# Kernel optimization log

Measured on AMD Instinct MI355X. Metric: run time of the kernel, lower is better.

Reference implementation:

```python
import jax, jax.numpy as jnp
import numpy as np

N_PANO, N_FP = 50000, 10000
D_IN, D_FP, HID, OUT = 128, 64, 128, 64
E_PP, E_PF = 800000, 50000


def _gat(x_src, x_dst, src, dst, Ws, Wd, a_s, a_d, b, n_dst):
    # PyG GATConv (heads=1, add_self_loops=False, bipartite lin_src/lin_dst)
    hs = x_src @ Ws                      # [Ns, C]
    hd = x_dst @ Wd                      # [Nd, C]
    es = hs @ a_s                        # [Ns]
    ed = hd @ a_d                        # [Nd]
    e = jax.nn.leaky_relu(es[src] + ed[dst], negative_slope=0.2)  # [E]
    m = jax.ops.segment_max(e, dst, num_segments=n_dst)
    ex = jnp.exp(e - m[dst])
    den = jax.ops.segment_sum(ex, dst, num_segments=n_dst)
    alpha = ex / den[dst]                # segment softmax over incoming edges
    out = jax.ops.segment_sum(hs[src] * alpha[:, None], dst, num_segments=n_dst)
    return out + b


def setup_inputs() -> dict:
    key = jax.random.key(0)
    ks = jax.random.split(key, 32)
    s_in = 1.0 / np.sqrt(D_IN)
    s_hid = 1.0 / np.sqrt(HID)
    s_fp = 1.0 / np.sqrt(D_FP)
    inp = {
        "x_pano": jax.random.normal(ks[0], (N_PANO, D_IN), jnp.float32),
        "x_fp": jax.random.normal(ks[1], (N_FP, D_FP), jnp.float32),
        # layer 0 (in = D_IN)
        "Ws0": jax.random.normal(ks[2], (D_IN, HID)) * s_in,
        "Wd0": jax.random.normal(ks[3], (D_IN, HID)) * s_in,
        "as0": jax.random.normal(ks[4], (HID,)) * 0.1,
        "ad0": jax.random.normal(ks[5], (HID,)) * 0.1,
        "b0": jnp.zeros((HID,), jnp.float32),
        "Lw0": jax.random.normal(ks[6], (D_IN, HID)) * s_in,
        "Lb0": jnp.zeros((HID,), jnp.float32),
        # layer 1 (in = HID)
        "Ws1": jax.random.normal(ks[7], (HID, HID)) * s_hid,
        "Wd1": jax.random.normal(ks[8], (HID, HID)) * s_hid,
        "as1": jax.random.normal(ks[9], (HID,)) * 0.1,
        "ad1": jax.random.normal(ks[10], (HID,)) * 0.1,
        "b1": jnp.zeros((HID,), jnp.float32),
        "Lw1": jax.random.normal(ks[11], (HID, HID)) * s_hid,
        "Lb1": jnp.zeros((HID,), jnp.float32),
        # translate conv pano -> footprint
        "Wts": jax.random.normal(ks[12], (HID, OUT)) * s_hid,
        "Wtd": jax.random.normal(ks[13], (D_FP, OUT)) * s_fp,
        "ats": jax.random.normal(ks[14], (OUT,)) * 0.1,
        "atd": jax.random.normal(ks[15], (OUT,)) * 0.1,
        "bt": jnp.zeros((OUT,), jnp.float32),
        "edge_pp": jax.random.randint(ks[16], (2, E_PP), 0, N_PANO),
        "edge_pf_src": jax.random.randint(ks[17], (E_PF,), 0, N_PANO),
        "edge_pf_dst": jax.random.randint(ks[18], (E_PF,), 0, N_FP),
    }
    return inp


def reference(x_pano, x_fp, Ws0, Wd0, as0, ad0, b0, Lw0, Lb0,
              Ws1, Wd1, as1, ad1, b1, Lw1, Lb1,
              Wts, Wtd, ats, atd, bt,
              edge_pp, edge_pf_src, edge_pf_dst):
    src, dst = edge_pp[0], edge_pp[1]
    layer_params = [(Ws0, Wd0, as0, ad0, b0, Lw0, Lb0),
                    (Ws1, Wd1, as1, ad1, b1, Lw1, Lb1)]
    h = x_pano
    for (Ws, Wd, a_s, a_d, b, Lw, Lb) in layer_params:
        conv = _gat(h, h, src, dst, Ws, Wd, a_s, a_d, b, N_PANO)
        h = jax.nn.relu(conv + h @ Lw + Lb)
    # HeteroConv with single relation + aggr='sum' == the bipartite conv output
    out_fp = _gat(h, x_fp, edge_pf_src, edge_pf_dst, Wts, Wtd, ats, atd, bt, N_FP)
    return out_fp
```

## Files before the change

kernel.cpp:

```cpp
#include <hip/hip_runtime.h>
#include <hip/hip_bf16.h>
#include <math.h>

#define N_PANO 50000
#define N_FP   10000
#define N_UNI  60000
#define HID    128
#define OUT_C  64
#define E_PP   800000
#define E_PF   50000
#define E_UNI  850000
#define NBKT   235
#define EPB    4096

typedef unsigned short ushort_t;
typedef unsigned int uint_t;
typedef __attribute__((ext_vector_type(8))) short short8;
typedef __attribute__((ext_vector_type(4))) float f32x4;

static inline int cdiv(int a, int b) { return (a + b - 1) / b; }

__device__ inline ushort_t f2bf(float x) {
    __hip_bfloat16 h = __float2bfloat16(x);
    return *reinterpret_cast<ushort_t*>(&h);
}
__device__ inline float bfu2f(ushort_t u) {
    return __uint_as_float(((uint_t)u) << 16);
}
__device__ inline float bflo(uint_t u) { return __uint_as_float((u & 0xffffu) << 16); }
__device__ inline float bfhi(uint_t u) { return __uint_as_float(u & 0xffff0000u); }
__device__ inline f32x4 mfma16(short8 a, short8 b, f32x4 c) {
    return __builtin_amdgcn_mfma_f32_16x16x32_bf16(a, b, c, 0, 0, 0);
}

__global__ __launch_bounds__(256) void zero_i32(int* p, int n) {
    int i = blockIdx.x * 256 + threadIdx.x;
    if (i < n) p[i] = 0;
}

__global__ __launch_bounds__(256) void bucket_count(const int* __restrict__ pp_dst,
                                                    const int* __restrict__ pf_dst,
                                                    int* __restrict__ bcnt) {
    __shared__ int hist[NBKT];
    const int tid = threadIdx.x;
    const int e0 = blockIdx.x * EPB;
    for (int t = tid; t < NBKT; t += 256) hist[t] = 0;
    __syncthreads();
    #pragma unroll
    for (int u = 0; u < EPB / 256; ++u) {
        int e = e0 + u * 256 + tid;
        int d = -1;
        if (e < E_PP) d = pp_dst[e];
        else if (e < E_UNI) d = N_PANO + pf_dst[e - E_PP];
        if (d >= 0) atomicAdd(&hist[d >> 8], 1);
    }
    __syncthreads();
    for (int t = tid; t < NBKT; t += 256)
        if (hist[t] > 0) atomicAdd(&bcnt[t * 16], hist[t]);
}

__global__ __launch_bounds__(256) void bucket_scan(const int* __restrict__ bcnt,
                                                   int* __restrict__ base, int* __restrict__ bcur) {
    __shared__ int wsum[4];
    int tid = threadIdx.x, lane = tid & 63, wid = tid >> 6;
    int v = (tid < NBKT) ? bcnt[tid * 16] : 0;
    int incl = v;
    #pragma unroll
    for (int off = 1; off < 64; off <<= 1) {
        int t = __shfl_up(incl, off, 64);
        if (lane >= off) incl += t;
    }
    if (lane == 63) wsum[wid] = incl;
    __syncthreads();
    if (tid == 0) {
        int run = 0;
        #pragma unroll
        for (int w = 0; w < 4; ++w) { int t = wsum[w]; wsum[w] = run; run += t; }
    }
    __syncthreads();
    int excl = wsum[wid] + incl - v;
    if (tid < NBKT) { base[tid] = excl; bcur[tid * 16] = excl; }
    if (tid == NBKT) base[NBKT] = E_UNI;
}

__global__ __launch_bounds__(256) void bucket_scatter_uni(const int* __restrict__ pp_src,
                                                          const int* __restrict__ pp_dst,
                                                          const int* __restrict__ pf_src,
                                                          const int* __restrict__ pf_dst,
                                                          int* __restrict__ bcur, int2* __restrict__ tmp) {
    __shared__ int hist[NBKT];
    __shared__ int base[NBKT];
    const int tid = threadIdx.x;
    const int e0 = blockIdx.x * EPB;
    for (int t = tid; t < NBKT; t += 256) hist[t] = 0;
    __syncthreads();
    int d[16], s[16];
    #pragma unroll
    for (int u = 0; u < 16; ++u) {
        int e = e0 + u * 256 + tid;
        if (e < E_PP)       { d[u] = pp_dst[e];                 s[u] = pp_src[e]; }
        else if (e < E_UNI) { d[u] = N_PANO + pf_dst[e - E_PP]; s[u] = pf_src[e - E_PP]; }
        else d[u] = -1;
        if (d[u] >= 0) atomicAdd(&hist[d[u] >> 8], 1);
    }
    __syncthreads();
    for (int t = tid; t < NBKT; t += 256) {
        int c = hist[t];
        base[t] = (c > 0) ? atomicAdd(&bcur[t * 16], c) : 0;
        hist[t] = 0;
    }
    __syncthreads();
    #pragma unroll
    for (int u = 0; u < 16; ++u) {
        if (d[u] >= 0) {
            int b = d[u] >> 8;
            int p = base[b] + atomicAdd(&hist[b], 1);
            tmp[p] = make_int2(s[u], d[u]);
        }
    }
}

__global__ __launch_bounds__(256) void bucket_fine_sort(const int2* __restrict__ tmp,
                                                        const int* __restrict__ base,
                                                        int* __restrict__ ptr, int* __restrict__ col) {
    __shared__ int hist[256];
    __shared__ int wsum[4];
    const int b = blockIdx.x, tid = threadIdx.x, lane = tid & 63, wid = tid >> 6;
    const int B0 = base[b], B1 = base[b + 1];
    hist[tid] = 0;
    __syncthreads();
    for (int e = B0 + tid; e < B1; e += 256) atomicAdd(&hist[tmp[e].y & 255], 1);
    __syncthreads();
    int v = hist[tid];
    int incl = v;
    #pragma unroll
    for (int off = 1; off < 64; off <<= 1) {
        int t = __shfl_up(incl, off, 64);
        if (lane >= off) incl += t;
    }
    if (lane == 63) wsum[wid] = incl;
    __syncthreads();
    if (tid == 0) {
        int run = 0;
        #pragma unroll
        for (int w = 0; w < 4; ++w) { int t = wsum[w]; wsum[w] = run; run += t; }
    }
    __syncthreads();
    int excl = wsum[wid] + incl - v;
    int dg = b * 256 + tid;
    if (dg < N_UNI) ptr[dg] = B0 + excl;
    if (b == NBKT - 1 && tid == 0) ptr[N_UNI] = E_UNI;
    hist[tid] = excl;
    __syncthreads();
    for (int e = B0 + tid; e < B1; e += 256) {
        int2 ed = tmp[e];
        int p = B0 + atomicAdd(&hist[ed.y & 255], 1);
        col[p] = ed.x;
    }
}

__global__ __launch_bounds__(64) void wed_all(const float* __restrict__ Wd0, const float* __restrict__ ad0,
                                              const float* __restrict__ Wd1, const float* __restrict__ ad1,
                                              const float* __restrict__ Wtd, const float* __restrict__ atd,
                                              float* __restrict__ o0, float* __restrict__ o1,
                                              float* __restrict__ ot) {
    int bid = blockIdx.x, lane = threadIdx.x;
    const float* W; const float* a; float* o; int r, C;
    if (bid < 128)      { W = Wd0; a = ad0; o = o0; r = bid;       C = 128; }
    else if (bid < 256) { W = Wd1; a = ad1; o = o1; r = bid - 128; C = 128; }
    else                { W = Wtd; a = atd; o = ot; r = bid - 256; C = 64;  }
    float s = 0.f;
    for (int j = lane; j < C; j += 64) s += W[r * C + j] * a[j];
    #pragma unroll
    for (int off = 32; off; off >>= 1) s += __shfl_down(s, off, 64);
    if (lane == 0) o[r] = s;
}

__global__ __launch_bounds__(256) void wconv(const float* __restrict__ Ws0, const float* __restrict__ Lw0,
                                             const float* __restrict__ Ws1, const float* __restrict__ Lw1,
                                             const float* __restrict__ Wts,
                                             ushort_t* s0, ushort_t* l0, ushort_t* s1, ushort_t* l1,
                                             ushort_t* ts) {
    int i = blockIdx.x * 256 + threadIdx.x;
    const float* W; ushort_t* oh;
    int d, NIc, Cc;
    if (i < 65536) {
        int m = i >> 14; d = i & 16383;
        W = (m == 0) ? Ws0 : (m == 1) ? Lw0 : (m == 2) ? Ws1 : Lw1;
        oh = (m == 0) ? s0 : (m == 1) ? l0 : (m == 2) ? s1 : l1;
        NIc = 8; Cc = 128;
    } else if (i < 73728) {
        d = i - 65536; W = Wts; oh = ts;
        NIc = 4; Cc = 64;
    } else return;
    int j = d & 7, l = (d >> 3) & 63;
    int kcl = (d >> 9) & 1;
    int ni = (d >> 10) & (NIc - 1);
    int p = d >> (10 + (NIc == 8 ? 3 : 2));
    int kc = p * 2 + kcl;
    int n = ni * 16 + (l & 15);
    int k = kc * 32 + (l >> 4) * 8 + j;
    oh[d] = f2bf(W[k * Cc + n]);
}

template <int CN, bool DUAL, bool FP32IN>
__global__ __launch_bounds__(256, 2) void gemm_mfma(const float* __restrict__ Xf,
                                                 const ushort_t* __restrict__ Xh,
                                                 const ushort_t* __restrict__ W1, const ushort_t* __restrict__ W2,
                                                 ushort_t* __restrict__ Y1, ushort_t* __restrict__ Y2,
                                                 const float* __restrict__ avec, float* __restrict__ evec,
                                                 const float* __restrict__ wed, float* __restrict__ edv,
                                                 int N) {
    constexpr int NI = CN / 16;
    constexpr int NMAT = DUAL ? 2 : 1;
    constexpr int SLAB = NI * 1024;
    __shared__ ushort_t Bsh[NMAT * SLAB];
    const int tid = threadIdx.x;
    const int w = tid >> 6, l = tid & 63;
    const int col = l & 15, q = l >> 4;
    const int row0 = blockIdx.x * 128 + w * 32;
    f32x4 acc1[2][NI];
    f32x4 acc2[2][DUAL ? NI : 1];
    #pragma unroll
    for (int m = 0; m < 2; ++m)
        #pragma unroll
        for (int ni = 0; ni < NI; ++ni)
            #pragma unroll
            for (int r = 0; r < 4; ++r) acc1[m][ni][r] = 0.f;
    if (DUAL) {
        #pragma unroll
        for (int m = 0; m < 2; ++m)
            #pragma unroll
            for (int ni = 0; ni < NI; ++ni)
                #pragma unroll
                for (int r = 0; r < 4; ++r) acc2[m][ni][r] = 0.f;
    }
    float ped[2] = {0.f, 0.f};

    #pragma unroll
    for (int p = 0; p < 2; ++p) {
        if (p) __syncthreads();
        {
            const uint4* src1 = (const uint4*)W1 + p * (SLAB / 8);
            uint4* dst1 = (uint4*)&Bsh[0];
            #pragma unroll
            for (int f = tid; f < SLAB / 8; f += 256) dst1[f] = src1[f];
            if (DUAL) {
                const uint4* src2 = (const uint4*)W2 + p * (SLAB / 8);
                uint4* dst2 = (uint4*)&Bsh[SLAB];
                #pragma unroll
                for (int f = tid; f < SLAB / 8; f += 256) dst2[f] = src2[f];
            }
        }
        __syncthreads();
        #pragma unroll
        for (int kcl = 0; kcl < 2; ++kcl) {
            const int kc = p * 2 + kcl;
            const int k0 = kc * 32 + q * 8;
            short8 Ah[2];
            #pragma unroll
            for (int m = 0; m < 2; ++m) {
                const int arow = row0 + m * 16 + col;
                if (FP32IN) {
                    float xv[8];
                    if (arow < N) {
                        float4 a0 = *(const float4*)&Xf[(size_t)arow * 128 + k0];
                        float4 a1 = *(const float4*)&Xf[(size_t)arow * 128 + k0 + 4];
                        xv[0] = a0.x; xv[1] = a0.y; xv[2] = a0.z; xv[3] = a0.w;
                        xv[4] = a1.x; xv[5] = a1.y; xv[6] = a1.z; xv[7] = a1.w;
                    } else {
                        #pragma unroll
                        for (int j = 0; j < 8; ++j) xv[j] = 0.f;
                    }
                    #pragma unroll
                    for (int j = 0; j < 8; ++j) Ah[m][j] = (short)f2bf(xv[j]);
                    if (wed) {
                        float4 w0 = *(const float4*)&wed[k0];
                        float4 w1 = *(const float4*)&wed[k0 + 4];
                        ped[m] += xv[0] * w0.x + xv[1] * w0.y + xv[2] * w0.z + xv[3] * w0.w
                                + xv[4] * w1.x + xv[5] * w1.y + xv[6] * w1.z + xv[7] * w1.w;
                    }
                } else {
                    if (arow < N) {
                        Ah[m] = *(const short8*)&Xh[(size_t)arow * 128 + k0];
                    } else {
                        #pragma unroll
                        for (int j = 0; j < 8; ++j) Ah[m][j] = 0;
                    }
                    if (wed) {
                        float4 w0 = *(const float4*)&wed[k0];
                        float4 w1 = *(const float4*)&wed[k0 + 4];
                        float wv[8] = {w0.x, w0.y, w0.z, w0.w, w1.x, w1.y, w1.z, w1.w};
                        #pragma unroll
                        for (int j = 0; j < 8; ++j)
                            ped[m] += bfu2f((ushort_t)Ah[m][j]) * wv[j];
                    }
                }
            }
            #pragma unroll
            for (int ni = 0; ni < NI; ++ni) {
                const int lb = ((ni * 2 + kcl) * 64 + l) * 8;
                short8 B1 = *(const short8*)&Bsh[lb];
                #pragma unroll
                for (int m = 0; m < 2; ++m) acc1[m][ni] = mfma16(Ah[m], B1, acc1[m][ni]);
                if (DUAL) {
                    short8 B2 = *(const short8*)&Bsh[SLAB + lb];
                    #pragma unroll
                    for (int m = 0; m < 2; ++m) acc2[m][ni] = mfma16(Ah[m], B2, acc2[m][ni]);
                }
            }
        }
    }

    #pragma unroll
    for (int m = 0; m < 2; ++m) {
        #pragma unroll
        for (int ni = 0; ni < NI; ++ni) {
            #pragma unroll
            for (int r = 0; r < 4; ++r) {
                int mrow = row0 + m * 16 + q * 4 + r;
                if (mrow < N) {
                    Y1[(size_t)mrow * CN + ni * 16 + col] = f2bf(acc1[m][ni][r]);
                    if (DUAL) Y2[(size_t)mrow * CN + ni * 16 + col] = f2bf(acc2[m][ni][r]);
                }
            }
        }
    }
    float av[NI];
    #pragma unroll
    for (int ni = 0; ni < NI; ++ni) av[ni] = avec[ni * 16 + col];
    #pragma unroll
    for (int m = 0; m < 2; ++m) {
        #pragma unroll
        for (int r = 0; r < 4; ++r) {
            float pp = 0.f;
            #pragma unroll
            for (int ni = 0; ni < NI; ++ni) pp += acc1[m][ni][r] * av[ni];
            pp += __shfl_xor(pp, 1, 64);
            pp += __shfl_xor(pp, 2, 64);
            pp += __shfl_xor(pp, 4, 64);
            pp += __shfl_xor(pp, 8, 64);
            int mrow = row0 + m * 16 + q * 4 + r;
            if (col == 0 && mrow < N) evec[mrow] = pp;
        }
    }
    if (wed) {
        #pragma unroll
        for (int m = 0; m < 2; ++m) {
            ped[m] += __shfl_xor(ped[m], 16, 64);
            ped[m] += __shfl_xor(ped[m], 32, 64);
            int arow = row0 + m * 16 + col;
            if (q == 0 && arow < N) edv[arow] = ped[m];
        }
    }
}

template <int K>
__global__ __launch_bounds__(256) void matvec_k(const float* __restrict__ X, const float* __restrict__ v,
                                                float* __restrict__ y, int N) {
    int lane = threadIdx.x & 63, wid = threadIdx.x >> 6;
    int node = blockIdx.x * 4 + wid;
    if (node >= N) return;
    float s = X[node * K + lane] * v[lane];
    if (K > 64) s += X[node * K + 64 + lane] * v[64 + lane];
    #pragma unroll
    for (int off = 32; off; off >>= 1) s += __shfl_down(s, off, 64);
    if (lane == 0) y[node] = s;
}

__global__ __launch_bounds__(256) void agg_pano6(const int* __restrict__ ptr, const int* __restrict__ col,
                                                 const float* __restrict__ es, const float* __restrict__ ed,
                                                 const ushort_t* __restrict__ hsb, const ushort_t* __restrict__ linb,
                                                 const float* __restrict__ b, const float* __restrict__ Lb,
                                                 uint_t* __restrict__ hh, int N) {
    int lane = threadIdx.x & 63, wid = threadIdx.x >> 6;
    int node = blockIdx.x * 4 + wid;
    if (node >= N) return;
    int beg = ptr[node], end = ptr[node + 1];
    float edn = ed[node];
    const int half = lane >> 5, hl = lane & 31;
    float a0 = 0.f, a1 = 0.f, a2 = 0.f, a3 = 0.f, denp = 0.f;
    for (int base = beg; base < end; base += 64) {
        int m = min(64, end - base);
        int s = 0;
        float wgt = 0.f;
        if (lane < m) {
            s = col[base + lane];
            float e = es[s] + edn;
            e = fmaxf(e, 0.2f * e);
            wgt = __expf(e);
        }
        denp += wgt;
        int mp = (m + 1) & ~1;
        int t = 0;
        for (; t + 8 <= mp; t += 8) {
            int i0 = t + half, i1 = t + 2 + half, i2 = t + 4 + half, i3 = t + 6 + half;
            int s0 = __shfl(s, i0, 64), s1 = __shfl(s, i1, 64);
            int s2 = __shfl(s, i2, 64), s3 = __shfl(s, i3, 64);
            float w0 = __shfl(wgt, i0, 64), w1 = __shfl(wgt, i1, 64);
            float w2 = __shfl(wgt, i2, 64), w3 = __shfl(wgt, i3, 64);
            uint2 h0 = *(const uint2*)&hsb[(size_t)s0 * 128 + hl * 4];
            uint2 h1 = *(const uint2*)&hsb[(size_t)s1 * 128 + hl * 4];
            uint2 h2 = *(const uint2*)&hsb[(size_t)s2 * 128 + hl * 4];
            uint2 h3 = *(const uint2*)&hsb[(size_t)s3 * 128 + hl * 4];
            a0 += w0 * bflo(h0.x) + w1 * bflo(h1.x) + w2 * bflo(h2.x) + w3 * bflo(h3.x);
            a1 += w0 * bfhi(h0.x) + w1 * bfhi(h1.x) + w2 * bfhi(h2.x) + w3 * bfhi(h3.x);
            a2 += w0 * bflo(h0.y) + w1 * bflo(h1.y) + w2 * bflo(h2.y) + w3 * bflo(h3.y);
            a3 += w0 * bfhi(h0.y) + w1 * bfhi(h1.y) + w2 * bfhi(h2.y) + w3 * bfhi(h3.y);
        }
        for (; t < mp; t += 2) {
            int i0 = t + half;
            int s0 = __shfl(s, i0, 64);
            float w0 = __shfl(wgt, i0, 64);
            uint2 h0 = *(const uint2*)&hsb[(size_t)s0 * 128 + hl * 4];
            a0 += w0 * bflo(h0.x);
            a1 += w0 * bfhi(h0.x);
            a2 += w0 * bflo(h0.y);
            a3 += w0 * bfhi(h0.y);
        }
    }
    a0 += __shfl_xor(a0, 32, 64);
    a1 += __shfl_xor(a1, 32, 64);
    a2 += __shfl_xor(a2, 32, 64);
    a3 += __shfl_xor(a3, 32, 64);
    float den = denp;
    #pragma unroll
    for (int off = 1; off < 64; off <<= 1) den += __shfl_xor(den, off, 64);
    float inv = (end > beg) ? (1.f / den) : 0.f;
    if (half == 0) {
        const ushort_t* lrow = linb + (size_t)node * 128;
        uint2 lv = *(const uint2*)&lrow[hl * 4];
        float4 bb = *(const float4*)&b[hl * 4];
        float4 lb4 = *(const float4*)&Lb[hl * 4];
        float o0 = fmaxf(a0 * inv + bb.x + bflo(lv.x) + lb4.x, 0.f);
        float o1 = fmaxf(a1 * inv + bb.y + bfhi(lv.x) + lb4.y, 0.f);
        float o2 = fmaxf(a2 * inv + bb.z + bflo(lv.y) + lb4.z, 0.f);
        float o3 = fmaxf(a3 * inv + bb.w + bfhi(lv.y) + lb4.w, 0.f);
        uint2 ov;
        ov.x = (uint_t)f2bf(o0) | ((uint_t)f2bf(o1) << 16);
        ov.y = (uint_t)f2bf(o2) | ((uint_t)f2bf(o3) << 16);
        *(uint2*)&hh[(size_t)node * 64 + hl * 2] = ov;
    }
}

__global__ __launch_bounds__(256) void agg_fp4(const int* __restrict__ ptr, const int* __restrict__ col,
                                               const float* __restrict__ es, const float* __restrict__ ed,
                                               const ushort_t* __restrict__ hsb, const float* __restrict__ bt,
                                               float* __restrict__ out, int N) {
    int lane = threadIdx.x & 63, wid = threadIdx.x >> 6;
    int node = blockIdx.x * 4 + wid;
    if (node >= N) return;
    int beg = ptr[node], end = ptr[node + 1];
    float edn = ed[node];
    float acc = 0.f, denp = 0.f;
    for (int base = beg; base < end; base += 64) {
        int m = min(64, end - base);
        int s = 0;
        float wgt = 0.f;
        if (lane < m) {
            s = col[base + lane];
            float e = es[s] + edn;
            e = fmaxf(e, 0.2f * e);
            wgt = __expf(e);
        }
        denp += wgt;
        int u = 0;
        for (; u + 4 <= m; u += 4) {
            int s0 = __shfl(s, u, 64), s1 = __shfl(s, u + 1, 64);
            int s2 = __shfl(s, u + 2, 64), s3 = __shfl(s, u + 3, 64);
            float w0 = __shfl(wgt, u, 64), w1 = __shfl(wgt, u + 1, 64);
            float w2 = __shfl(wgt, u + 2, 64), w3 = __shfl(wgt, u + 3, 64);
            float h0 = bfu2f(hsb[(size_t)s0 * 64 + lane]);
            float h1 = bfu2f(hsb[(size_t)s1 * 64 + lane]);
            float h2 = bfu2f(hsb[(size_t)s2 * 64 + lane]);
            float h3 = bfu2f(hsb[(size_t)s3 * 64 + lane]);
            acc += w0 * h0 + w1 * h1 + w2 * h2 + w3 * h3;
        }
        for (; u < m; ++u) {
            int su = __shfl(s, u, 64);
            float wu = __shfl(wgt, u, 64);
            acc += wu * bfu2f(hsb[(size_t)su * 64 + lane]);
        }
    }
    float den = denp;
    #pragma unroll
    for (int off = 1; off < 64; off <<= 1) den += __shfl_xor(den, off, 64);
    float inv = (end > beg) ? (1.f / den) : 0.f;
    out[(size_t)node * 64 + lane] = acc * inv + bt[lane];
}

extern "C" void kernel_launch(void* const* d_in, const int* in_sizes, int n_in,
                              void* d_out, int out_size, void* d_ws, size_t ws_size,
                              hipStream_t stream) {
    const float* x_pano = (const float*)d_in[0];
    const float* x_fp   = (const float*)d_in[1];
    const float* Ws0 = (const float*)d_in[2];
    const float* Wd0 = (const float*)d_in[3];
    const float* as0 = (const float*)d_in[4];
    const float* ad0 = (const float*)d_in[5];
    const float* b0  = (const float*)d_in[6];
    const float* Lw0 = (const float*)d_in[7];
    const float* Lb0 = (const float*)d_in[8];
    const float* Ws1 = (const float*)d_in[9];
    const float* Wd1 = (const float*)d_in[10];
    const float* as1 = (const float*)d_in[11];
    const float* ad1 = (const float*)d_in[12];
    const float* b1  = (const float*)d_in[13];
    const float* Lw1 = (const float*)d_in[14];
    const float* Lb1 = (const float*)d_in[15];
    const float* Wts = (const float*)d_in[16];
    const float* Wtd = (const float*)d_in[17];
    const float* ats = (const float*)d_in[18];
    const float* atd = (const float*)d_in[19];
    const float* bt  = (const float*)d_in[20];
    const int* edge_pp = (const int*)d_in[21];
    const int* pf_src  = (const int*)d_in[22];
    const int* pf_dst  = (const int*)d_in[23];
    float* out = (float*)d_out;

    char* wsp = (char*)d_ws;
    size_t off = 0;
    auto alloc = [&](size_t bytes) -> char* {
        char* p = wsp + off;
        off += (bytes + 255) & ~(size_t)255;
        return p;
    };
    ushort_t* hsb  = (ushort_t*)alloc(sizeof(ushort_t) * N_PANO * HID);
    ushort_t* linb = (ushort_t*)alloc(sizeof(ushort_t) * N_PANO * HID);
    uint_t* hh     = (uint_t*)alloc(sizeof(uint_t) * N_PANO * 64);
    ushort_t* hstb = (ushort_t*)alloc(sizeof(ushort_t) * N_PANO * OUT_C);
    int2* tmp_e    = (int2*)alloc(sizeof(int2) * E_UNI);
    float* es   = (float*)alloc(sizeof(float) * N_PANO);
    float* ed   = (float*)alloc(sizeof(float) * N_PANO);
    float* edt  = (float*)alloc(sizeof(float) * N_FP);
    float* wed0 = (float*)alloc(sizeof(float) * HID);
    float* wed1 = (float*)alloc(sizeof(float) * HID);
    float* wedt = (float*)alloc(sizeof(float) * OUT_C);
    ushort_t* s0 = (ushort_t*)alloc(sizeof(ushort_t) * 128 * 128);
    ushort_t* l0 = (ushort_t*)alloc(sizeof(ushort_t) * 128 * 128);
    ushort_t* s1 = (ushort_t*)alloc(sizeof(ushort_t) * 128 * 128);
    ushort_t* l1 = (ushort_t*)alloc(sizeof(ushort_t) * 128 * 128);
    ushort_t* ts = (ushort_t*)alloc(sizeof(ushort_t) * 64 * 128);
    int* bcnt   = (int*)alloc(sizeof(int) * NBKT * 16);
    int* bcur   = (int*)alloc(sizeof(int) * NBKT * 16);
    int* bbase  = (int*)alloc(sizeof(int) * (NBKT + 1));
    int* P      = (int*)alloc(sizeof(int) * (N_UNI + 1));
    int* col_u  = (int*)alloc(sizeof(int) * E_UNI);

    const int* pp_src = edge_pp;
    const int* pp_dst = edge_pp + E_PP;

    zero_i32<<<cdiv(NBKT * 16, 256), 256, 0, stream>>>(bcnt, NBKT * 16);
    bucket_count<<<cdiv(E_UNI, EPB), 256, 0, stream>>>(pp_dst, pf_dst, bcnt);
    bucket_scan<<<1, 256, 0, stream>>>(bcnt, bbase, bcur);
    bucket_scatter_uni<<<cdiv(E_UNI, EPB), 256, 0, stream>>>(pp_src, pp_dst, pf_src, pf_dst, bcur, tmp_e);
    bucket_fine_sort<<<NBKT, 256, 0, stream>>>(tmp_e, bbase, P, col_u);

    wed_all<<<320, 64, 0, stream>>>(Wd0, ad0, Wd1, ad1, Wtd, atd, wed0, wed1, wedt);
    wconv<<<288, 256, 0, stream>>>(Ws0, Lw0, Ws1, Lw1, Wts, s0, l0, s1, l1, ts);

    const int gemm_grid = cdiv(N_PANO, 128);

    gemm_mfma<128, true, true><<<gemm_grid, 256, 0, stream>>>(
        x_pano, nullptr, s0, l0, hsb, linb, as0, es, wed0, ed, N_PANO);
    agg_pano6<<<cdiv(N_PANO, 4), 256, 0, stream>>>(P, col_u, es, ed, hsb, linb, b0, Lb0, hh, N_PANO);

    gemm_mfma<128, true, false><<<gemm_grid, 256, 0, stream>>>(
        nullptr, (const ushort_t*)hh, s1, l1, hsb, linb, as1, es, wed1, ed, N_PANO);
    agg_pano6<<<cdiv(N_PANO, 4), 256, 0, stream>>>(P, col_u, es, ed, hsb, linb, b1, Lb1, hh, N_PANO);

    gemm_mfma<64, false, false><<<gemm_grid, 256, 0, stream>>>(
        nullptr, (const ushort_t*)hh, ts, nullptr, hstb, nullptr, ats, es, nullptr, nullptr, N_PANO);
    matvec_k<64><<<cdiv(N_FP, 4), 256, 0, stream>>>(x_fp, wedt, edt, N_FP);
    agg_fp4<<<cdiv(N_FP, 4), 256, 0, stream>>>(P + N_PANO, col_u, es, edt, hstb, bt, out, N_FP);
}
```

Baseline: 282.3 us.

## Process two nodes per wave in pano aggregation and merge prep kernels

The pano aggregation kernel now assigns two destination nodes to each wavefront and interleaves their edge chunks. Each half-wave writes one node's output, which aims to raise memory-level parallelism and cut idle lanes on low-degree nodes. The two weight-prep kernels are merged into one launch. The footprint dst-score matvec is folded into the footprint aggregation kernel, removing one more launch. Handling two nodes per wave raises register pressure and adds serialization when the two nodes have very different degrees.

Measured after the change: 277.8 us. About the same (-1.6%).

```diff
diff --git a/kernel.cpp b/kernel.cpp
--- a/kernel.cpp
+++ b/kernel.cpp
@@ -159,48 +159,51 @@
     }
 }
 
-__global__ __launch_bounds__(64) void wed_all(const float* __restrict__ Wd0, const float* __restrict__ ad0,
+__global__ __launch_bounds__(256) void prep_k(const float* __restrict__ Ws0, const float* __restrict__ Lw0,
+                                              const float* __restrict__ Ws1, const float* __restrict__ Lw1,
+                                              const float* __restrict__ Wts,
+                                              const float* __restrict__ Wd0, const float* __restrict__ ad0,
                                               const float* __restrict__ Wd1, const float* __restrict__ ad1,
                                               const float* __restrict__ Wtd, const float* __restrict__ atd,
-                                              float* __restrict__ o0, float* __restrict__ o1,
-                                              float* __restrict__ ot) {
-    int bid = blockIdx.x, lane = threadIdx.x;
-    const float* W; const float* a; float* o; int r, C;
-    if (bid < 128)      { W = Wd0; a = ad0; o = o0; r = bid;       C = 128; }
-    else if (bid < 256) { W = Wd1; a = ad1; o = o1; r = bid - 128; C = 128; }
-    else                { W = Wtd; a = atd; o = ot; r = bid - 256; C = 64;  }
-    float s = 0.f;
-    for (int j = lane; j < C; j += 64) s += W[r * C + j] * a[j];
-    #pragma unroll
-    for (int off = 32; off; off >>= 1) s += __shfl_down(s, off, 64);
-    if (lane == 0) o[r] = s;
-}
-
-__global__ __launch_bounds__(256) void wconv(const float* __restrict__ Ws0, const float* __restrict__ Lw0,
-                                             const float* __restrict__ Ws1, const float* __restrict__ Lw1,
-                                             const float* __restrict__ Wts,
-                                             ushort_t* s0, ushort_t* l0, ushort_t* s1, ushort_t* l1,
-                                             ushort_t* ts) {
-    int i = blockIdx.x * 256 + threadIdx.x;
-    const float* W; ushort_t* oh;
-    int d, NIc, Cc;
-    if (i < 65536) {
-        int m = i >> 14; d = i & 16383;
-        W = (m == 0) ? Ws0 : (m == 1) ? Lw0 : (m == 2) ? Ws1 : Lw1;
-        oh = (m == 0) ? s0 : (m == 1) ? l0 : (m == 2) ? s1 : l1;
-        NIc = 8; Cc = 128;
-    } else if (i < 73728) {
-        d = i - 65536; W = Wts; oh = ts;
-        NIc = 4; Cc = 64;
-    } else return;
-    int j = d & 7, l = (d >> 3) & 63;
-    int kcl = (d >> 9) & 1;
-    int ni = (d >> 10) & (NIc - 1);
-    int p = d >> (10 + (NIc == 8 ? 3 : 2));
-    int kc = p * 2 + kcl;
-    int n = ni * 16 + (l & 15);
-    int k = kc * 32 + (l >> 4) * 8 + j;
-    oh[d] = f2bf(W[k * Cc + n]);
+                                              ushort_t* s0, ushort_t* l0, ushort_t* s1, ushort_t* l1,
+                                              ushort_t* ts,
+                                              float* wed0, float* wed1, float* wedt) {
+    const int blk = blockIdx.x, tid = threadIdx.x;
+    if (blk < 288) {
+        int i = blk * 256 + tid;
+        const float* W; ushort_t* oh;
+        int d, NIc, Cc;
+        if (i < 65536) {
+            int m = i >> 14; d = i & 16383;
+            W = (m == 0) ? Ws0 : (m == 1) ? Lw0 : (m == 2) ? Ws1 : Lw1;
+            oh = (m == 0) ? s0 : (m == 1) ? l0 : (m == 2) ? s1 : l1;
+            NIc = 8; Cc = 128;
+        } else if (i < 73728) {
+            d = i - 65536; W = Wts; oh = ts;
+            NIc = 4; Cc = 64;
+        } else return;
+        int j = d & 7, l = (d >> 3) & 63;
+        int kcl = (d >> 9) & 1;
+        int ni = (d >> 10) & (NIc - 1);
+        int p = d >> (10 + (NIc == 8 ? 3 : 2));
+        int kc = p * 2 + kcl;
+        int n = ni * 16 + (l & 15);
+        int k = kc * 32 + (l >> 4) * 8 + j;
+        oh[d] = f2bf(W[k * Cc + n]);
+    } else {
+        int r = (blk - 288) * 4 + (tid >> 6);
+        int lane = tid & 63;
+        const float* W; const float* a; float* o; int rr, C;
+        if (r < 128)      { W = Wd0; a = ad0; o = wed0; rr = r;       C = 128; }
+        else if (r < 256) { W = Wd1; a = ad1; o = wed1; rr = r - 128; C = 128; }
+        else if (r < 320) { W = Wtd; a = atd; o = wedt; rr = r - 256; C = 64;  }
+        else return;
+        float s = 0.f;
+        for (int j = lane; j < C; j += 64) s += W[rr * C + j] * a[j];
+        #pragma unroll
+        for (int off = 32; off; off >>= 1) s += __shfl_down(s, off, 64);
+        if (lane == 0) o[rr] = s;
+    }
 }
 
 template <int CN, bool DUAL, bool FP32IN>
@@ -355,87 +358,125 @@
     }
 }
 
-template <int K>
-__global__ __launch_bounds__(256) void matvec_k(const float* __restrict__ X, const float* __restrict__ v,
-                                                float* __restrict__ y, int N) {
-    int lane = threadIdx.x & 63, wid = threadIdx.x >> 6;
-    int node = blockIdx.x * 4 + wid;
-    if (node >= N) return;
-    float s = X[node * K + lane] * v[lane];
-    if (K > 64) s += X[node * K + 64 + lane] * v[64 + lane];
-    #pragma unroll
-    for (int off = 32; off; off >>= 1) s += __shfl_down(s, off, 64);
-    if (lane == 0) y[node] = s;
-}
-
-__global__ __launch_bounds__(256) void agg_pano6(const int* __restrict__ ptr, const int* __restrict__ col,
+__global__ __launch_bounds__(256) void agg_pano7(const int* __restrict__ ptr, const int* __restrict__ col,
                                                  const float* __restrict__ es, const float* __restrict__ ed,
                                                  const ushort_t* __restrict__ hsb, const ushort_t* __restrict__ linb,
                                                  const float* __restrict__ b, const float* __restrict__ Lb,
                                                  uint_t* __restrict__ hh, int N) {
     int lane = threadIdx.x & 63, wid = threadIdx.x >> 6;
-    int node = blockIdx.x * 4 + wid;
-    if (node >= N) return;
-    int beg = ptr[node], end = ptr[node + 1];
-    float edn = ed[node];
+    int nodeA = blockIdx.x * 8 + wid * 2;
+    if (nodeA >= N) return;
+    int nodeB = nodeA + 1;
+    bool hasB = nodeB < N;
+    int begA = ptr[nodeA], endA = ptr[nodeA + 1];
+    int endB = hasB ? ptr[nodeB + 1] : endA;
+    int begB = endA;
+    float ednA = ed[nodeA];
+    float ednB = hasB ? ed[nodeB] : 0.f;
     const int half = lane >> 5, hl = lane & 31;
-    float a0 = 0.f, a1 = 0.f, a2 = 0.f, a3 = 0.f, denp = 0.f;
-    for (int base = beg; base < end; base += 64) {
-        int m = min(64, end - base);
-        int s = 0;
-        float wgt = 0.f;
-        if (lane < m) {
-            s = col[base + lane];
-            float e = es[s] + edn;
+    float aA0 = 0.f, aA1 = 0.f, aA2 = 0.f, aA3 = 0.f, dA = 0.f;
+    float aB0 = 0.f, aB1 = 0.f, aB2 = 0.f, aB3 = 0.f, dB = 0.f;
+    int baseA = begA, baseB = begB;
+    while (baseA < endA || baseB < endB) {
+        int mA = endA - baseA; mA = mA < 0 ? 0 : (mA > 64 ? 64 : mA);
+        int mB = endB - baseB; mB = mB < 0 ? 0 : (mB > 64 ? 64 : mB);
+        int sA = 0, sB = 0;
+        float wA = 0.f, wB = 0.f;
+        if (lane < mA) {
+            sA = col[baseA + lane];
+            float e = es[sA] + ednA;
             e = fmaxf(e, 0.2f * e);
-            wgt = __expf(e);
-        }
-        denp += wgt;
-        int mp = (m + 1) & ~1;
-        int t = 0;
-        for (; t + 8 <= mp; t += 8) {
-            int i0 = t + half, i1 = t + 2 + half, i2 = t + 4 + half, i3 = t + 6 + half;
-            int s0 = __shfl(s, i0, 64), s1 = __shfl(s, i1, 64);
-            int s2 = __shfl(s, i2, 64), s3 = __shfl(s, i3, 64);
-            float w0 = __shfl(wgt, i0, 64), w1 = __shfl(wgt, i1, 64);
-            float w2 = __shfl(wgt, i2, 64), w3 = __shfl(wgt, i3, 64);
-            uint2 h0 = *(const uint2*)&hsb[(size_t)s0 * 128 + hl * 4];
-            uint2 h1 = *(const uint2*)&hsb[(size_t)s1 * 128 + hl * 4];
-            uint2 h2 = *(const uint2*)&hsb[(size_t)s2 * 128 + hl * 4];
-            uint2 h3 = *(const uint2*)&hsb[(size_t)s3 * 128 + hl * 4];
-            a0 += w0 * bflo(h0.x) + w1 * bflo(h1.x) + w2 * bflo(h2.x) + w3 * bflo(h3.x);
-            a1 += w0 * bfhi(h0.x) + w1 * bfhi(h1.x) + w2 * bfhi(h2.x) + w3 * bfhi(h3.x);
-            a2 += w0 * bflo(h0.y) + w1 * bflo(h1.y) + w2 * bflo(h2.y) + w3 * bflo(h3.y);
-            a3 += w0 * bfhi(h0.y) + w1 * bfhi(h1.y) + w2 * bfhi(h2.y) + w3 * bfhi(h3.y);
-        }
-        for (; t < mp; t += 2) {
-            int i0 = t + half;
-            int s0 = __shfl(s, i0, 64);
-            float w0 = __shfl(wgt, i0, 64);
-            uint2 h0 = *(const uint2*)&hsb[(size_t)s0 * 128 + hl * 4];
-            a0 += w0 * bflo(h0.x);
-            a1 += w0 * bfhi(h0.x);
-            a2 += w0 * bflo(h0.y);
-            a3 += w0 * bfhi(h0.y);
-        }
-    }
-    a0 += __shfl_xor(a0, 32, 64);
-    a1 += __shfl_xor(a1, 32, 64);
-    a2 += __shfl_xor(a2, 32, 64);
-    a3 += __shfl_xor(a3, 32, 64);
-    float den = denp;
-    #pragma unroll
-    for (int off = 1; off < 64; off <<= 1) den += __shfl_xor(den, off, 64);
-    float inv = (end > beg) ? (1.f / den) : 0.f;
-    if (half == 0) {
-        const ushort_t* lrow = linb + (size_t)node * 128;
-        uint2 lv = *(const uint2*)&lrow[hl * 4];
+            wA = __expf(e);
+        }
+        if (lane < mB) {
+            sB = col[baseB + lane];
+            float e = es[sB] + ednB;
+            e = fmaxf(e, 0.2f * e);
+            wB = __expf(e);
+        }
+        dA += wA; dB += wB;
+        {
+            int mp = (mA + 1) & ~1;
+            int t = 0;
+            for (; t + 8 <= mp; t += 8) {
+                int i0 = t + half, i1 = t + 2 + half, i2 = t + 4 + half, i3 = t + 6 + half;
+                int s0 = __shfl(sA, i0, 64), s1 = __shfl(sA, i1, 64);
+                int s2 = __shfl(sA, i2, 64), s3 = __shfl(sA, i3, 64);
+                float w0 = __shfl(wA, i0, 64), w1 = __shfl(wA, i1, 64);
+                float w2 = __shfl(wA, i2, 64), w3 = __shfl(wA, i3, 64);
+                uint2 h0 = *(const uint2*)&hsb[(size_t)s0 * 128 + hl * 4];
+                uint2 h1 = *(const uint2*)&hsb[(size_t)s1 * 128 + hl * 4];
+                uint2 h2 = *(const uint2*)&hsb[(size_t)s2 * 128 + hl * 4];
+                uint2 h3 = *(const uint2*)&hsb[(size_t)s3 * 128 + hl * 4];
+                aA0 += w0 * bflo(h0.x) + w1 * bflo(h1.x) + w2 * bflo(h2.x) + w3 * bflo(h3.x);
+                aA1 += w0 * bfhi(h0.x) + w1 * bfhi(h1.x) + w2 * bfhi(h2.x) + w3 * bfhi(h3.x);
+                aA2 += w0 * bflo(h0.y) + w1 * bflo(h1.y) + w2 * bflo(h2.y) + w3 * bflo(h3.y);
+                aA3 += w0 * bfhi(h0.y) + w1 * bfhi(h1.y) + w2 * bfhi(h2.y) + w3 * bfhi(h3.y);
+            }
+            for (; t < mp; t += 2) {
+                int i0 = t + half;
+                int s0 = __shfl(sA, i0, 64);
+                float w0 = __shfl(wA, i0, 64);
+                uint2 h0 = *(const uint2*)&hsb[(size_t)s0 * 128 + hl * 4];
+                aA0 += w0 * bflo(h0.x);
+                aA1 += w0 * bfhi(h0.x);
+                aA2 += w0 * bflo(h0.y);
+                aA3 += w0 * bfhi(h0.y);
+            }
+        }
+        {
+            int mp = (mB + 1) & ~1;
+            int t = 0;
+            for (; t + 8 <= mp; t += 8) {
+                int i0 = t + half, i1 = t + 2 + half, i2 = t + 4 + half, i3 = t + 6 + half;
+                int s0 = __shfl(sB, i0, 64), s1 = __shfl(sB, i1, 64);
+                int s2 = __shfl(sB, i2, 64), s3 = __shfl(sB, i3, 64);
+                float w0 = __shfl(wB, i0, 64), w1 = __shfl(wB, i1, 64);
+                float w2 = __shfl(wB, i2, 64), w3 = __shfl(wB, i3, 64);
+                uint2 h0 = *(const uint2*)&hsb[(size_t)s0 * 128 + hl * 4];
+                uint2 h1 = *(const uint2*)&hsb[(size_t)s1 * 128 + hl * 4];
+                uint2 h2 = *(const uint2*)&hsb[(size_t)s2 * 128 + hl * 4];
+                uint2 h3 = *(const uint2*)&hsb[(size_t)s3 * 128 + hl * 4];
+                aB0 += w0 * bflo(h0.x) + w1 * bflo(h1.x) + w2 * bflo(h2.x) + w3 * bflo(h3.x);
+                aB1 += w0 * bfhi(h0.x) + w1 * bfhi(h1.x) + w2 * bfhi(h2.x) + w3 * bfhi(h3.x);
+                aB2 += w0 * bflo(h0.y) + w1 * bflo(h1.y) + w2 * bflo(h2.y) + w3 * bflo(h3.y);
+                aB3 += w0 * bfhi(h0.y) + w1 * bfhi(h1.y) + w2 * bfhi(h2.y) + w3 * bfhi(h3.y);
+            }
+            for (; t < mp; t += 2) {
+                int i0 = t + half;
+                int s0 = __shfl(sB, i0, 64);
+                float w0 = __shfl(wB, i0, 64);
+                uint2 h0 = *(const uint2*)&hsb[(size_t)s0 * 128 + hl * 4];
+                aB0 += w0 * bflo(h0.x);
+                aB1 += w0 * bfhi(h0.x);
+                aB2 += w0 * bflo(h0.y);
+                aB3 += w0 * bfhi(h0.y);
+            }
+        }
+        baseA += 64; baseB += 64;
+    }
+    aA0 += __shfl_xor(aA0, 32, 64); aA1 += __shfl_xor(aA1, 32, 64);
+    aA2 += __shfl_xor(aA2, 32, 64); aA3 += __shfl_xor(aA3, 32, 64);
+    aB0 += __shfl_xor(aB0, 32, 64); aB1 += __shfl_xor(aB1, 32, 64);
+    aB2 += __shfl_xor(aB2, 32, 64); aB3 += __shfl_xor(aB3, 32, 64);
+    #pragma unroll
+    for (int off = 1; off < 64; off <<= 1) dA += __shfl_xor(dA, off, 64);
+    #pragma unroll
+    for (int off = 1; off < 64; off <<= 1) dB += __shfl_xor(dB, off, 64);
+    float invA = (endA > begA) ? (1.f / dA) : 0.f;
+    float invB = (endB > begB) ? (1.f / dB) : 0.f;
+    int node = half ? nodeB : nodeA;
+    if (half == 0 || hasB) {
+        float v0 = half ? aB0 : aA0, v1 = half ? aB1 : aA1;
+        float v2 = half ? aB2 : aA2, v3 = half ? aB3 : aA3;
+        float inv = half ? invB : invA;
+        uint2 lv = *(const uint2*)&linb[(size_t)node * 128 + hl * 4];
         float4 bb = *(const float4*)&b[hl * 4];
         float4 lb4 = *(const float4*)&Lb[hl * 4];
-        float o0 = fmaxf(a0 * inv + bb.x + bflo(lv.x) + lb4.x, 0.f);
-        float o1 = fmaxf(a1 * inv + bb.y + bfhi(lv.x) + lb4.y, 0.f);
-        float o2 = fmaxf(a2 * inv + bb.z + bflo(lv.y) + lb4.z, 0.f);
-        float o3 = fmaxf(a3 * inv + bb.w + bfhi(lv.y) + lb4.w, 0.f);
+        float o0 = fmaxf(v0 * inv + bb.x + bflo(lv.x) + lb4.x, 0.f);
+        float o1 = fmaxf(v1 * inv + bb.y + bfhi(lv.x) + lb4.y, 0.f);
+        float o2 = fmaxf(v2 * inv + bb.z + bflo(lv.y) + lb4.z, 0.f);
+        float o3 = fmaxf(v3 * inv + bb.w + bfhi(lv.y) + lb4.w, 0.f);
         uint2 ov;
         ov.x = (uint_t)f2bf(o0) | ((uint_t)f2bf(o1) << 16);
         ov.y = (uint_t)f2bf(o2) | ((uint_t)f2bf(o3) << 16);
@@ -443,15 +484,18 @@
     }
 }
 
-__global__ __launch_bounds__(256) void agg_fp4(const int* __restrict__ ptr, const int* __restrict__ col,
-                                               const float* __restrict__ es, const float* __restrict__ ed,
+__global__ __launch_bounds__(256) void agg_fp5(const int* __restrict__ ptr, const int* __restrict__ col,
+                                               const float* __restrict__ es, const float* __restrict__ x_fp,
+                                               const float* __restrict__ wedt,
                                                const ushort_t* __restrict__ hsb, const float* __restrict__ bt,
                                                float* __restrict__ out, int N) {
     int lane = threadIdx.x & 63, wid = threadIdx.x >> 6;
     int node = blockIdx.x * 4 + wid;
     if (node >= N) return;
     int beg = ptr[node], end = ptr[node + 1];
-    float edn = ed[node];
+    float edn = x_fp[(size_t)node * 64 + lane] * wedt[lane];
+    #pragma unroll
+    for (int off = 1; off < 64; off <<= 1) edn += __shfl_xor(edn, off, 64);
     float acc = 0.f, denp = 0.f;
     for (int base = beg; base < end; base += 64) {
         int m = min(64, end - base);
@@ -532,7 +576,6 @@
     int2* tmp_e    = (int2*)alloc(sizeof(int2) * E_UNI);
     float* es   = (float*)alloc(sizeof(float) * N_PANO);
     float* ed   = (float*)alloc(sizeof(float) * N_PANO);
-    float* edt  = (float*)alloc(sizeof(float) * N_FP);
     float* wed0 = (float*)alloc(sizeof(float) * HID);
     float* wed1 = (float*)alloc(sizeof(float) * HID);
     float* wedt = (float*)alloc(sizeof(float) * OUT_C);
@@ -556,21 +599,20 @@
     bucket_scatter_uni<<<cdiv(E_UNI, EPB), 256, 0, stream>>>(pp_src, pp_dst, pf_src, pf_dst, bcur, tmp_e);
     bucket_fine_sort<<<NBKT, 256, 0, stream>>>(tmp_e, bbase, P, col_u);
 
-    wed_all<<<320, 64, 0, stream>>>(Wd0, ad0, Wd1, ad1, Wtd, atd, wed0, wed1, wedt);
-    wconv<<<288, 256, 0, stream>>>(Ws0, Lw0, Ws1, Lw1, Wts, s0, l0, s1, l1, ts);
+    prep_k<<<368, 256, 0, stream>>>(Ws0, Lw0, Ws1, Lw1, Wts, Wd0, ad0, Wd1, ad1, Wtd, atd,
+                                    s0, l0, s1, l1, ts, wed0, wed1, wedt);
 
     const int gemm_grid = cdiv(N_PANO, 128);
 
     gemm_mfma<128, true, true><<<gemm_grid, 256, 0, stream>>>(
         x_pano, nullptr, s0, l0, hsb, linb, as0, es, wed0, ed, N_PANO);
-    agg_pano6<<<cdiv(N_PANO, 4), 256, 0, stream>>>(P, col_u, es, ed, hsb, linb, b0, Lb0, hh, N_PANO);
+    agg_pano7<<<cdiv(N_PANO, 8), 256, 0, stream>>>(P, col_u, es, ed, hsb, linb, b0, Lb0, hh, N_PANO);
 
     gemm_mfma<128, true, false><<<gemm_grid, 256, 0, stream>>>(
         nullptr, (const ushort_t*)hh, s1, l1, hsb, linb, as1, es, wed1, ed, N_PANO);
-    agg_pano6<<<cdiv(N_PANO, 4), 256, 0, stream>>>(P, col_u, es, ed, hsb, linb, b1, Lb1, hh, N_PANO);
+    agg_pano7<<<cdiv(N_PANO, 8), 256, 0, stream>>>(P, col_u, es, ed, hsb, linb, b1, Lb1, hh, N_PANO);
 
     gemm_mfma<64, false, false><<<gemm_grid, 256, 0, stream>>>(
         nullptr, (const ushort_t*)hh, ts, nullptr, hstb, nullptr, ats, es, nullptr, nullptr, N_PANO);
-    matvec_k<64><<<cdiv(N_FP, 4), 256, 0, stream>>>(x_fp, wedt, edt, N_FP);
-    agg_fp4<<<cdiv(N_FP, 4), 256, 0, stream>>>(P + N_PANO, col_u, es, edt, hstb, bt, out, N_FP);
-}
+    agg_fp5<<<cdiv(N_FP, 4), 256, 0, stream>>>(P + N_PANO, col_u, es, x_fp, wedt, hstb, bt, out, N_FP);
+}
```
